# Kernel optimization log

Measured on AMD Instinct MI355X. Metric: run time of the kernel, lower is better.

## Reference

```python
import jax, jax.numpy as jnp
import numpy as np

B, N, V, T = 16, 1024, 4096, 8


def _lsa(cost):
    """Jonker-Volgenant linear sum assignment on a square [n,n] cost matrix.
    Returns (row_ind, col_ind) minimizing cost[row, col].sum(). Equivalent to
    scipy.optimize.linear_sum_assignment for square matrices."""
    n = cost.shape[0]
    INF = np.inf
    u = np.zeros(n + 1)
    v = np.zeros(n + 1)
    p = np.zeros(n + 1, dtype=np.int64)    # p[j] = row assigned to column j (1-based)
    way = np.zeros(n + 1, dtype=np.int64)
    for i in range(1, n + 1):
        p[0] = i
        j0 = 0
        minv = np.full(n + 1, INF)
        used = np.zeros(n + 1, dtype=bool)
        while True:
            used[j0] = True
            i0 = p[j0]
            free = ~used
            free[0] = False
            cur = cost[i0 - 1, :] - u[i0] - v[1:]
            upd = free[1:] & (cur < minv[1:])
            minv[1:][upd] = cur[upd]
            way[1:][upd] = j0
            j1 = int(np.argmin(np.where(free[1:], minv[1:], INF))) + 1
            delta = minv[j1]
            u[p[used]] += delta
            v[used] -= delta
            minv[~used] -= delta
            j0 = j1
            if p[j0] == 0:
                break
        while j0:
            j1 = way[j0]
            p[j0] = p[j1]
            j0 = j1
    col_of_row = np.empty(n, dtype=np.int64)
    for j in range(1, n + 1):
        col_of_row[p[j] - 1] = j - 1
    return np.arange(n), col_of_row


def _compute_assignment(lp_np, gt_np, types_np, mask_np):
    """For each (sample, node_type) group of masked nodes, Hungarian-match
    positions to gt tokens. Returns flat (batch_idx, pos_idx, tok_idx) of all
    matched pairs. Mirrors the original type-wise padded loop (k==1 is identity)."""
    Bn = lp_np.shape[0]
    b_l, p_l, t_l = [], [], []
    for t in np.unique(types_np):
        for b in range(Bn):
            idx = np.nonzero((types_np[b] == t) & mask_np[b])[0]
            k = idx.size
            if k == 0:
                continue
            g = gt_np[b, idx]
            if k == 1:
                r = np.zeros(1, dtype=np.int64)
                c = np.zeros(1, dtype=np.int64)
            else:
                cost = -lp_np[b, idx][:, g]  # [k, k]
                r, c = _lsa(cost)
            b_l.append(np.full(k, b, dtype=np.int64))
            p_l.append(idx[r])
            t_l.append(g[c])
    return np.concatenate(b_l), np.concatenate(p_l), np.concatenate(t_l)


def setup_inputs() -> dict:
    key = jax.random.key(0)
    k1, k2, k3, k4 = jax.random.split(key, 4)
    logits = jax.random.normal(k1, (B, N, V), dtype=jnp.float32)
    gt_tokens = jax.random.randint(k2, (B, N), 0, V)
    node_types = jax.random.randint(k3, (B, N), 0, T)
    mask_positions = jax.random.randint(k4, (B, N), 0, 2).astype(bool)
    return {"logits": logits, "gt_tokens": gt_tokens,
            "node_types": node_types, "mask_positions": mask_positions}


def reference(logits, gt_tokens, node_types, mask_positions):
    # Dense log-softmax over vocab (the memory-bound bulk of the op).
    log_probs = jax.nn.log_softmax(logits, axis=-1)
    # Assignment is computed on detached values (matches .detach() in original).
    b_idx, p_idx, t_idx = _compute_assignment(
        np.asarray(jax.lax.stop_gradient(log_probs)),
        np.asarray(gt_tokens), np.asarray(node_types), np.asarray(mask_positions))
    total = b_idx.shape[0]  # total matched (masked) tokens
    sel = log_probs[jnp.asarray(b_idx), jnp.asarray(p_idx), jnp.asarray(t_idx)]
    # avg_loss = sum_b(loss_per_sample*count)/total_count == sum of matched NLL / total
    return -sel.sum() / jnp.asarray(total, sel.dtype)
```

## Files before the change

### kernel.cpp

```cpp
#include <hip/hip_runtime.h>
#include <math.h>

#define BB 16
#define NN 1024
#define VV 4096
#define TT 8
#define NG (BB*TT)
#define KMAX 124
#define STRIDE 124

__device__ __forceinline__ float wave_max(float v){
  #pragma unroll
  for (int off = 32; off; off >>= 1) v = fmaxf(v, __shfl_down(v, off));
  return v;
}
__device__ __forceinline__ float wave_sum(float v){
  #pragma unroll
  for (int off = 32; off; off >>= 1) v += __shfl_down(v, off);
  return v;
}

__device__ __forceinline__ unsigned fkey(float f){
  unsigned b = __float_as_uint(f);
  return b ^ ((unsigned)((int)b >> 31) | 0x80000000u);
}
__device__ __forceinline__ float inv_fkey(unsigned u){
  unsigned b = (u & 0x80000000u) ? (u ^ 0x80000000u) : ~u;
  return __uint_as_float(b);
}

__device__ __forceinline__ unsigned dpp_min64(unsigned x){
  unsigned t;
  t = (unsigned)__builtin_amdgcn_update_dpp(-1, (int)x, 0x111, 0xF, 0xF, false); x = x < t ? x : t;
  t = (unsigned)__builtin_amdgcn_update_dpp(-1, (int)x, 0x112, 0xF, 0xF, false); x = x < t ? x : t;
  t = (unsigned)__builtin_amdgcn_update_dpp(-1, (int)x, 0x114, 0xF, 0xF, false); x = x < t ? x : t;
  t = (unsigned)__builtin_amdgcn_update_dpp(-1, (int)x, 0x118, 0xF, 0xF, false); x = x < t ? x : t;
  t = (unsigned)__builtin_amdgcn_update_dpp(-1, (int)x, 0x142, 0xF, 0xF, false); x = x < t ? x : t;
  t = (unsigned)__builtin_amdgcn_update_dpp(-1, (int)x, 0x143, 0xF, 0xF, false); x = x < t ? x : t;
  return x;
}

__global__ __launch_bounds__(256) void k_lse(const float* __restrict__ logits,
                                             const unsigned char* __restrict__ raw,
                                             float* __restrict__ lse){
  int row = blockIdx.x;
  int tid = threadIdx.x;
  __shared__ int probe_nz;
  if (tid == 0) probe_nz = 0;
  __syncthreads();
  uchar4 pv = ((const uchar4*)raw)[tid];
  if (pv.y | pv.z | pv.w) atomicOr(&probe_nz, 1);
  __syncthreads();
  bool bool_layout = (probe_nz != 0);
  int mv = bool_layout ? (int)raw[row] : ((const int*)raw)[row];
  if (mv == 0){ if (tid == 0) lse[row] = 0.f; return; }

  const float4* x = (const float4*)(logits + (size_t)row * VV);
  float4 a = x[tid], b = x[tid+256], c = x[tid+512], d = x[tid+768];
  float m = fmaxf(fmaxf(fmaxf(fmaxf(a.x,a.y),fmaxf(a.z,a.w)),
                        fmaxf(fmaxf(b.x,b.y),fmaxf(b.z,b.w))),
                  fmaxf(fmaxf(fmaxf(c.x,c.y),fmaxf(c.z,c.w)),
                        fmaxf(fmaxf(d.x,d.y),fmaxf(d.z,d.w))));
  __shared__ float red[8];
  float wm = wave_max(m);
  int wid = tid >> 6;
  if ((tid & 63) == 0) red[wid] = wm;
  __syncthreads();
  if (tid == 0) red[4] = fmaxf(fmaxf(red[0],red[1]), fmaxf(red[2],red[3]));
  __syncthreads();
  float M = red[4];
  float s = __expf(a.x-M)+__expf(a.y-M)+__expf(a.z-M)+__expf(a.w-M)
          + __expf(b.x-M)+__expf(b.y-M)+__expf(b.z-M)+__expf(b.w-M)
          + __expf(c.x-M)+__expf(c.y-M)+__expf(c.z-M)+__expf(c.w-M)
          + __expf(d.x-M)+__expf(d.y-M)+__expf(d.z-M)+__expf(d.w-M);
  float ws = wave_sum(s);
  __syncthreads();
  if ((tid & 63) == 0) red[wid] = ws;
  __syncthreads();
  if (tid == 0) lse[row] = M + __logf(red[0]+red[1]+red[2]+red[3]);
}

__global__ __launch_bounds__(64) void k_jv(const float* __restrict__ logits,
                                           const int* __restrict__ types,
                                           const int* __restrict__ gt,
                                           const unsigned char* __restrict__ raw,
                                           int* __restrict__ kcnt,
                                           float* __restrict__ gval){
  __shared__ float Cm[KMAX*STRIDE];
  __shared__ float u_l[KMAX+1];
  __shared__ int   p_l[KMAX+1];
  __shared__ int   way_l[KMAX+1];
  __shared__ int   rowown[KMAX];
  __shared__ int   listA[KMAX];
  __shared__ int   listB[KMAX];
  int g = blockIdx.x, b = g >> 3, t = g & 7, lane = threadIdx.x;
  unsigned long long lm = (1ull << lane) - 1ull;

  int local = 0;
  const uchar4* r4 = (const uchar4*)raw;
  #pragma unroll
  for (int r = 0; r < 4; r++){ uchar4 u = r4[lane + 64*r]; local |= (u.y | u.z | u.w); }
  bool bool_layout = (__ballot(local != 0) != 0ull);
  const int* rawi = (const int*)raw;
  int base = 0;
  for (int r = 0; r < NN/64; r++){
    int pos = r*64 + lane, o = b*NN + pos;
    int mv = bool_layout ? (int)raw[o] : rawi[o];
    bool pred = (types[o] == t) && (mv != 0);
    unsigned long long ball = __ballot(pred);
    int dst = base + __popcll(ball & lm);
    if (pred && dst < KMAX){ way_l[dst] = pos; listA[dst] = gt[o]; }
    base += __popcll(ball);
  }
  int k = (base > KMAX) ? KMAX : base;
  if (lane == 0) kcnt[g] = k;
  if (k == 0){ if (lane == 0) gval[g] = 0.f; return; }

  int col0 = lane + 1, col1 = lane + 65;
  bool a0 = (col0 <= k), a1 = (col1 <= k);
  int gc0 = a0 ? listA[lane]      : 0;
  int gc1 = a1 ? listA[lane + 64] : 0;

  u_l[col0] = 0.f; p_l[col0] = 0;
  if (col1 <= KMAX){ u_l[col1] = 0.f; p_l[col1] = 0; }
  if (lane == 0){ u_l[0] = 0.f; p_l[0] = 0; }
  rowown[lane] = -1;
  if (lane + 64 < KMAX) rowown[lane+64] = -1;
  __syncthreads();

  const size_t rowbase = (size_t)b * NN;
  for (int i = 0; i < k; i += 8){
    float xs0[8], xs1[8]; int rr[8];
    #pragma unroll
    for (int s = 0; s < 8; s++){
      int r = i + s; r = (r < k) ? r : (k - 1); rr[s] = r;
      const float* q = logits + (rowbase + way_l[r]) * VV;
      xs0[s] = q[gc0]; xs1[s] = q[gc1];
    }
    #pragma unroll
    for (int s = 0; s < 8; s++){
      Cm[rr[s]*STRIDE + lane]      = -xs0[s];
      Cm[rr[s]*STRIDE + 64 + lane] = -xs1[s];
    }
  }
  __syncthreads();

  float v0 = 0.f, v1 = 0.f;
  int ra0 = -1, ra1 = -1;
  if (a0){ float m = INFINITY; int rm = 0;
    for (int i = 0; i < k; i++){ float c = Cm[i*STRIDE + lane]; if (c < m){ m = c; rm = i; } }
    v0 = m; ra0 = rm; }
  if (a1){ float m = INFINITY; int rm = 0;
    for (int i = 0; i < k; i++){ float c = Cm[i*STRIDE + 64 + lane]; if (c < m){ m = c; rm = i; } }
    v1 = m; ra1 = rm; }
  if (a0){ if (atomicCAS(&rowown[ra0], -1, col0) == -1) p_l[col0] = ra0 + 1; }
  if (a1){ if (atomicCAS(&rowown[ra1], -1, col1) == -1) p_l[col1] = ra1 + 1; }
  __syncthreads();

  bool f0 = (lane < k)    && (rowown[lane]    == -1);
  bool f1 = (lane+64 < k) && (rowown[lane+64] == -1);
  unsigned long long B0 = __ballot(f0), B1 = __ballot(f1);
  int n0 = __popcll(B0);
  if (f0) listA[__popcll(B0 & lm)]      = lane + 1;
  if (f1) listA[n0 + __popcll(B1 & lm)] = lane + 65;
  int nCur = n0 + __popcll(B1);
  __syncthreads();

  int* curL = listA; int* nxtL = listB;
  for (int pass = 0; pass < 3; pass++){
    int nNxt = 0;
    for (int fr = 0; fr < nCur; fr++){
      int row = curL[fr];
      int off = (row - 1) * STRIDE;
      float rc0 = a0 ? (Cm[off + lane]      - v0) : INFINITY;
      float rc1 = a1 ? (Cm[off + 64 + lane] - v1) : INFINITY;
      unsigned k0 = fkey(rc0), k1 = fkey(rc1);
      unsigned kk = k0 < k1 ? k0 : k1;
      unsigned m1 = (unsigned)__builtin_amdgcn_readlane((int)dpp_min64(kk), 63);
      int cand = (k0 == m1) ? col0 : ((k1 == m1) ? col1 : 0);
      unsigned long long bl1 = __ballot(cand != 0);
      int ow1 = __ffsll(bl1) - 1;
      int j1 = __builtin_amdgcn_readlane(cand, ow1);
      float u1 = inv_fkey(m1);
      unsigned k0b = (col0 == j1) ? 0xFFFFFFFFu : k0;
      unsigned k1b = (col1 == j1) ? 0xFFFFFFFFu : k1;
      unsigned kkb = k0b < k1b ? k0b : k1b;
      unsigned m2 = (unsigned)__builtin_amdgcn_readlane((int)dpp_min64(kkb), 63);
      float u2 = inv_fkey(m2);
      int jt = j1;
      if (u1 < u2){
        if (col0 == j1) v0 -= (u2 - u1);
        if (col1 == j1) v1 -= (u2 - u1);
      } else {
        int own1 = p_l[j1];
        if (own1 != 0){
          int cand2 = (k0b == m2) ? col0 : ((k1b == m2) ? col1 : 0);
          unsigned long long bl2 = __ballot(cand2 != 0);
          int ow2 = __ffsll(bl2) - 1;
          jt = __builtin_amdgcn_readlane(cand2, ow2);
        }
      }
      int iprev = p_l[jt];
      if (lane == 0){ p_l[jt] = row; u_l[row] = u2; }
      if (iprev != 0){ if (lane == 0) nxtL[nNxt] = iprev; nNxt++; }
      __syncthreads();
    }
    int* tmp = curL; curL = nxtL; nxtL = tmp;
    nCur = nNxt;
  }

  for (int fr = 0; fr < nCur; fr++){
    int irow = curL[fr];
    int rp0 = a0 ? p_l[col0] : 0;
    int rp1 = a1 ? p_l[col1] : 0;
    float rpu0 = (rp0 > 0) ? u_l[rp0] : 0.f;
    float rpu1 = (rp1 > 0) ? u_l[rp1] : 0.f;
    int off = (irow - 1) * STRIDE;
    float dist0 = a0 ? (Cm[off + lane]      - v0) : INFINITY;
    float dist1 = a1 ? (Cm[off + 64 + lane] - v1) : INFINITY;
    int way0 = 0, way1 = 0;
    bool used0 = false, used1 = false;
    int j_end; float delta_end;
    while (true){
      unsigned q0 = (a0 && !used0) ? ((fkey(dist0) & 0xFFFFFF80u) | (unsigned)(col0-1)) : 0xFFFFFFFFu;
      unsigned q1 = (a1 && !used1) ? ((fkey(dist1) & 0xFFFFFF80u) | (unsigned)(col1-1)) : 0xFFFFFFFFu;
      unsigned key = q0 < q1 ? q0 : q1;
      unsigned kmin = (unsigned)__builtin_amdgcn_readlane((int)dpp_min64(key), 63);
      int j1 = (int)(kmin & 127u) + 1;
      int owner = (j1-1) & 63, slot = (j1-1) >> 6;
      float dsel  = slot ? dist1 : dist0;
      int   psel  = slot ? rp1   : rp0;
      float pusel = slot ? rpu1  : rpu0;
      float delta = __uint_as_float((unsigned)__builtin_amdgcn_readlane(__float_as_int(dsel), owner));
      int   i0    = __builtin_amdgcn_readlane(psel, owner);
      float pu    = __uint_as_float((unsigned)__builtin_amdgcn_readlane(__float_as_int(pusel), owner));
      used0 |= (j1 == col0);
      used1 |= (j1 == col1);
      if (i0 == 0){ j_end = j1; delta_end = delta; break; }
      float bse = delta - pu;
      int o2 = (i0 - 1) * STRIDE;
      float c0 = Cm[o2 + lane];
      float c1 = Cm[o2 + 64 + lane];
      float nd0 = bse + c0 - v0;
      float nd1 = bse + c1 - v1;
      if (a0 && !used0 && (nd0 < dist0)){ dist0 = nd0; way0 = j1; }
      if (a1 && !used1 && (nd1 < dist1)){ dist1 = nd1; way1 = j1; }
    }
    if (used0){ float adj = delta_end - dist0; v0 -= adj; u_l[rp0] = rpu0 + adj; }
    if (used1){ float adj = delta_end - dist1; v1 -= adj; u_l[rp1] = rpu1 + adj; }
    if (lane == 0) u_l[irow] = delta_end;
    if (a0) way_l[col0] = way0;
    if (a1) way_l[col1] = way1;
    __syncthreads();
    int j0 = j_end;
    while (true){
      int jw = way_l[j0];
      int pr = p_l[jw];
      int pw = (jw == 0) ? irow : pr;
      if (lane == 0) p_l[j0] = pw;
      if (jw == 0) break;
      j0 = jw;
    }
    __syncthreads();
  }

  __syncthreads();
  float acc = 0.f;
  if (a0) acc += Cm[(p_l[col0]-1)*STRIDE + lane];
  if (a1) acc += Cm[(p_l[col1]-1)*STRIDE + 64 + lane];
  acc = wave_sum(acc);
  if (lane == 0) gval[g] = -acc;
}

__global__ __launch_bounds__(256) void k_final(const float* __restrict__ lse,
                                               const int* __restrict__ kcnt,
                                               const float* __restrict__ gval,
                                               float* __restrict__ out){
  __shared__ double sd[256];
  __shared__ double sg[256];
  __shared__ int    si[256];
  int tid = threadIdx.x;
  double s = 0.0, gs = 0.0; int c = 0;
  for (int i = tid; i < BB*NN; i += 256) s += (double)lse[i];
  for (int i = tid; i < NG; i += 256){ gs += (double)gval[i]; c += kcnt[i]; }
  sd[tid] = s; sg[tid] = gs; si[tid] = c;
  __syncthreads();
  for (int off = 128; off; off >>= 1){
    if (tid < off){ sd[tid] += sd[tid+off]; sg[tid] += sg[tid+off]; si[tid] += si[tid+off]; }
    __syncthreads();
  }
  if (tid == 0) out[0] = (float)((sd[0] - sg[0]) / (double)si[0]);
}

extern "C" void kernel_launch(void* const* d_in, const int* in_sizes, int n_in,
                              void* d_out, int out_size, void* d_ws, size_t ws_size,
                              hipStream_t stream) {
  const float* logits = (const float*)d_in[0];
  const int*   gt     = (const int*)d_in[1];
  const int*   types  = (const int*)d_in[2];
  const unsigned char* maskraw = (const unsigned char*)d_in[3];
  float* out = (float*)d_out;

  char* w = (char*)d_ws;
  float* lse  = (float*)w;  w += (size_t)BB*NN*4;
  int*   kcnt = (int*)w;    w += 1024;
  float* gval = (float*)w;  w += 1024;

  k_lse  <<<BB*NN, 256, 0, stream>>>(logits, maskraw, lse);
  k_jv   <<<NG,     64, 0, stream>>>(logits, types, gt, maskraw, kcnt, gval);
  k_final<<<1,     256, 0, stream>>>(lse, kcnt, gval, out);
}
```

Before: 459.9 us.

## Fuse log-sum-exp and assignment kernels into one launch with single-wave LSE rows

Merges the per-row log-sum-exp kernel into the Hungarian assignment kernel as extra blocks, so the long-running assignment blocks (scheduled first) overlap with the bandwidth-bound LSE work instead of running after it. Each LSE row is now reduced by one 64-lane wave holding 16 float4 values in registers, using xor shuffles with no shared-memory barriers. The trade-offs are higher register pressure per LSE block and a shared-memory footprint inherited by all blocks of the fused kernel, which may reduce LSE occupancy.

```diff
diff --git a/kernel.cpp b/kernel.cpp
--- a/kernel.cpp
+++ b/kernel.cpp
@@ -9,11 +9,6 @@
 #define KMAX 124
 #define STRIDE 124
 
-__device__ __forceinline__ float wave_max(float v){
-  #pragma unroll
-  for (int off = 32; off; off >>= 1) v = fmaxf(v, __shfl_down(v, off));
-  return v;
-}
 __device__ __forceinline__ float wave_sum(float v){
   #pragma unroll
   for (int off = 32; off; off >>= 1) v += __shfl_down(v, off);
@@ -40,52 +35,43 @@
   return x;
 }
 
-__global__ __launch_bounds__(256) void k_lse(const float* __restrict__ logits,
+__global__ __launch_bounds__(64) void k_main(const float* __restrict__ logits,
+                                             const int* __restrict__ types,
+                                             const int* __restrict__ gt,
                                              const unsigned char* __restrict__ raw,
+                                             int* __restrict__ kcnt,
+                                             float* __restrict__ gval,
                                              float* __restrict__ lse){
-  int row = blockIdx.x;
-  int tid = threadIdx.x;
-  __shared__ int probe_nz;
-  if (tid == 0) probe_nz = 0;
-  __syncthreads();
-  uchar4 pv = ((const uchar4*)raw)[tid];
-  if (pv.y | pv.z | pv.w) atomicOr(&probe_nz, 1);
-  __syncthreads();
-  bool bool_layout = (probe_nz != 0);
-  int mv = bool_layout ? (int)raw[row] : ((const int*)raw)[row];
-  if (mv == 0){ if (tid == 0) lse[row] = 0.f; return; }
-
-  const float4* x = (const float4*)(logits + (size_t)row * VV);
-  float4 a = x[tid], b = x[tid+256], c = x[tid+512], d = x[tid+768];
-  float m = fmaxf(fmaxf(fmaxf(fmaxf(a.x,a.y),fmaxf(a.z,a.w)),
-                        fmaxf(fmaxf(b.x,b.y),fmaxf(b.z,b.w))),
-                  fmaxf(fmaxf(fmaxf(c.x,c.y),fmaxf(c.z,c.w)),
-                        fmaxf(fmaxf(d.x,d.y),fmaxf(d.z,d.w))));
-  __shared__ float red[8];
-  float wm = wave_max(m);
-  int wid = tid >> 6;
-  if ((tid & 63) == 0) red[wid] = wm;
-  __syncthreads();
-  if (tid == 0) red[4] = fmaxf(fmaxf(red[0],red[1]), fmaxf(red[2],red[3]));
-  __syncthreads();
-  float M = red[4];
-  float s = __expf(a.x-M)+__expf(a.y-M)+__expf(a.z-M)+__expf(a.w-M)
-          + __expf(b.x-M)+__expf(b.y-M)+__expf(b.z-M)+__expf(b.w-M)
-          + __expf(c.x-M)+__expf(c.y-M)+__expf(c.z-M)+__expf(c.w-M)
-          + __expf(d.x-M)+__expf(d.y-M)+__expf(d.z-M)+__expf(d.w-M);
-  float ws = wave_sum(s);
-  __syncthreads();
-  if ((tid & 63) == 0) red[wid] = ws;
-  __syncthreads();
-  if (tid == 0) lse[row] = M + __logf(red[0]+red[1]+red[2]+red[3]);
-}
-
-__global__ __launch_bounds__(64) void k_jv(const float* __restrict__ logits,
-                                           const int* __restrict__ types,
-                                           const int* __restrict__ gt,
-                                           const unsigned char* __restrict__ raw,
-                                           int* __restrict__ kcnt,
-                                           float* __restrict__ gval){
+  int lane = threadIdx.x;
+
+  if (blockIdx.x >= NG){
+    int row = blockIdx.x - NG;
+    uchar4 pv = ((const uchar4*)raw)[lane];
+    bool bool_layout = (__ballot((pv.y | pv.z | pv.w) != 0) != 0ull);
+    int mv = bool_layout ? (int)raw[row] : ((const int*)raw)[row];
+    if (mv == 0){ if (lane == 0) lse[row] = 0.f; return; }
+
+    const float4* x = (const float4*)(logits + (size_t)row * VV);
+    float4 v[16];
+    #pragma unroll
+    for (int i = 0; i < 16; i++) v[i] = x[lane + 64*i];
+    float m = -INFINITY;
+    #pragma unroll
+    for (int i = 0; i < 16; i++)
+      m = fmaxf(m, fmaxf(fmaxf(v[i].x, v[i].y), fmaxf(v[i].z, v[i].w)));
+    #pragma unroll
+    for (int off = 32; off; off >>= 1) m = fmaxf(m, __shfl_xor(m, off));
+    float s = 0.f;
+    #pragma unroll
+    for (int i = 0; i < 16; i++)
+      s += __expf(v[i].x - m) + __expf(v[i].y - m)
+         + __expf(v[i].z - m) + __expf(v[i].w - m);
+    #pragma unroll
+    for (int off = 32; off; off >>= 1) s += __shfl_xor(s, off);
+    if (lane == 0) lse[row] = m + __logf(s);
+    return;
+  }
+
   __shared__ float Cm[KMAX*STRIDE];
   __shared__ float u_l[KMAX+1];
   __shared__ int   p_l[KMAX+1];
@@ -93,7 +79,7 @@
   __shared__ int   rowown[KMAX];
   __shared__ int   listA[KMAX];
   __shared__ int   listB[KMAX];
-  int g = blockIdx.x, b = g >> 3, t = g & 7, lane = threadIdx.x;
+  int g = blockIdx.x, b = g >> 3, t = g & 7;
   unsigned long long lm = (1ull << lane) - 1ull;
 
   int local = 0;
@@ -306,7 +292,6 @@
   int*   kcnt = (int*)w;    w += 1024;
   float* gval = (float*)w;  w += 1024;
 
-  k_lse  <<<BB*NN, 256, 0, stream>>>(logits, maskraw, lse);
-  k_jv   <<<NG,     64, 0, stream>>>(logits, types, gt, maskraw, kcnt, gval);
-  k_final<<<1,     256, 0, stream>>>(lse, kcnt, gval, out);
-}
+  k_main <<<NG + BB*NN, 64, 0, stream>>>(logits, types, gt, maskraw, kcnt, gval, lse);
+  k_final<<<1, 256, 0, stream>>>(lse, kcnt, gval, out);
+}
```

New measurement: 431.4 us. -6.2%, faster.
